# Kernel tuning notes

Hardware: AMD Instinct MI355X
Metric: run time of the kernel (lower is better)

Reference implementation:

```python
import jax, jax.numpy as jnp
import numpy as np

B, S, D, H, E = 2, 2048, 1024, 2048, 8


def setup_inputs() -> dict:
    key = jax.random.key(0)
    ks = jax.random.split(key, 5)
    scale_in = 0.02
    x = jax.random.normal(ks[0], (B, S, D), dtype=jnp.float32)
    Wr = jax.random.normal(ks[1], (D, E), dtype=jnp.float32) * scale_in
    br = jnp.zeros((E,), dtype=jnp.float32)
    W1 = jax.random.normal(ks[2], (E, D, H), dtype=jnp.float32) * (1.0 / np.sqrt(D))
    b1 = jnp.zeros((E, H), dtype=jnp.float32)
    W2 = jax.random.normal(ks[3], (E, H, D), dtype=jnp.float32) * (1.0 / np.sqrt(H))
    b2 = jnp.zeros((E, D), dtype=jnp.float32)
    return {"x": x, "Wr": Wr, "br": br, "W1": W1, "b1": b1, "W2": W2, "b2": b2, "k": 2}


def reference(x, Wr, br, W1, b1, W2, b2, k):
    # Router: top-k logits, softmax over the k selected logits
    logits = x @ Wr + br                       # [B,S,E]
    top_v, top_i = jax.lax.top_k(logits, k)    # [B,S,k]
    scores = jax.nn.softmax(top_v, axis=-1)    # [B,S,k]

    # Dense all-expert MLP (reference combine): [B,S,E,*]
    h = jax.nn.relu(jnp.einsum('bsd,edh->bseh', x, W1) + b1[None, None])
    eo = jnp.einsum('bseh,ehd->bsed', h, W2) + b2[None, None]  # [B,S,E,D]

    # Gather the k selected experts per token and combine with scores
    sel = jnp.take_along_axis(eo, top_i[..., None], axis=2)   # [B,S,k,D]
    out = jnp.sum(scores[..., None] * sel, axis=2)             # [B,S,D]
    return out
```

## Files before the change

kernel.cpp:

```cpp
#include <hip/hip_runtime.h>
#include <hip/hip_bf16.h>

#define TOKENS 4096
#define DDIM 1024
#define HDIM 2048
#define NEXP 8
#define NASSIGN 8192
#define MAX_TILES 80

typedef __attribute__((ext_vector_type(8))) __bf16 bf16x8;
typedef __attribute__((ext_vector_type(4))) float f32x4;
typedef __attribute__((ext_vector_type(4))) unsigned short u16x4;

__device__ __forceinline__ unsigned short f2bf(float f) {
    unsigned int u = __builtin_bit_cast(unsigned int, f);
    u += 0x7fffu + ((u >> 16) & 1u);
    return (unsigned short)(u >> 16);
}

__global__ __launch_bounds__(256) void router_kernel(
    const float* __restrict__ x, const float* __restrict__ Wr, const float* __restrict__ br,
    unsigned short* __restrict__ x_bf, int* __restrict__ topk_e, float* __restrict__ topk_s,
    float* __restrict__ out)
{
    {
        float4* o4 = (float4*)(out + (long)blockIdx.x * 4 * DDIM);
        const float4 z = {0.f, 0.f, 0.f, 0.f};
        for (int i = threadIdx.x; i < DDIM; i += 256) o4[i] = z;
    }
    const int t = blockIdx.x * 4 + (threadIdx.x >> 6);
    const int lane = threadIdx.x & 63;
    const float* xr = x + (long)t * DDIM;
    unsigned short* xo = x_bf + (long)t * DDIM;
    float acc[8] = {0.f,0.f,0.f,0.f,0.f,0.f,0.f,0.f};
    for (int it = 0; it < DDIM / 64; ++it) {
        const int d = it * 64 + lane;
        const float xv = xr[d];
        xo[d] = f2bf(xv);
        const float4 w0 = *(const float4*)(Wr + d * 8);
        const float4 w1 = *(const float4*)(Wr + d * 8 + 4);
        acc[0] += xv * w0.x; acc[1] += xv * w0.y; acc[2] += xv * w0.z; acc[3] += xv * w0.w;
        acc[4] += xv * w1.x; acc[5] += xv * w1.y; acc[6] += xv * w1.z; acc[7] += xv * w1.w;
    }
#pragma unroll
    for (int e = 0; e < 8; ++e) {
        float v = acc[e];
        for (int off = 32; off > 0; off >>= 1) v += __shfl_down(v, off, 64);
        acc[e] = v;
    }
    if (lane == 0) {
        float lg[8];
#pragma unroll
        for (int e = 0; e < 8; ++e) lg[e] = acc[e] + br[e];
        int i0 = 0; float v0 = lg[0];
#pragma unroll
        for (int e = 1; e < 8; ++e) if (lg[e] > v0) { v0 = lg[e]; i0 = e; }
        int i1 = -1; float v1 = -3.4e38f;
#pragma unroll
        for (int e = 0; e < 8; ++e) if (e != i0 && lg[e] > v1) { v1 = lg[e]; i1 = e; }
        const float e1 = expf(v1 - v0);
        const float inv = 1.f / (1.f + e1);
        topk_e[t * 2]     = i0; topk_s[t * 2]     = inv;
        topk_e[t * 2 + 1] = i1; topk_s[t * 2 + 1] = e1 * inv;
    }
}

__global__ __launch_bounds__(1024) void build_lists_kernel(
    const int* __restrict__ topk_e, const float* __restrict__ topk_s,
    int* __restrict__ token_list, float* __restrict__ score_list, int* __restrict__ meta)
{
    __shared__ int cnt[NEXP];
    __shared__ int cur[NEXP];
    const int tid = threadIdx.x;
    const int lane = tid & 63;
    if (tid < NEXP) cnt[tid] = 0;
    __syncthreads();
    {
        int acc = 0;
        for (int it = 0; it < NASSIGN / 1024; ++it) {
            const int e = topk_e[it * 1024 + tid];
#pragma unroll
            for (int ee = 0; ee < NEXP; ++ee) {
                const unsigned long long m = __ballot(e == ee);
                if (lane == ee) acc += __popcll(m);
            }
        }
        if (lane < NEXP) atomicAdd(&cnt[lane], acc);
    }
    __syncthreads();
    if (tid == 0) {
        int accu = 0, ntile = 0;
        for (int e = 0; e < NEXP; ++e) {
            const int c = cnt[e];
            cur[e] = accu;
            for (int r = 0; r * 128 < c; ++r) {
                meta[1 + ntile] = e;
                meta[1 + MAX_TILES + ntile] = accu + r * 128;
                meta[1 + 2 * MAX_TILES + ntile] = (c - r * 128) < 128 ? (c - r * 128) : 128;
                ++ntile;
            }
            accu += c;
        }
        meta[0] = ntile;
    }
    __syncthreads();
    for (int it = 0; it < NASSIGN / 1024; ++it) {
        const int idx = it * 1024 + tid;
        const int e = topk_e[idx];
        const float s = topk_s[idx];
        int pos = 0;
#pragma unroll
        for (int ee = 0; ee < NEXP; ++ee) {
            const unsigned long long m = __ballot(e == ee);
            if (e == ee) {
                const int leader = __ffsll((long long)m) - 1;
                int wbase = 0;
                if (lane == leader) wbase = atomicAdd(&cur[ee], __popcll(m));
                wbase = __shfl(wbase, leader, 64);
                pos = wbase + __popcll(m & ((1ull << lane) - 1ull));
            }
        }
        token_list[pos] = idx >> 1;
        score_list[pos] = s;
    }
}

__global__ __launch_bounds__(256) void transpose_cvt_kernel(
    const float* __restrict__ W1, const float* __restrict__ W2,
    unsigned short* __restrict__ W1t, unsigned short* __restrict__ W2t)
{
    __shared__ unsigned short tile[64 * 68];
    const int z = blockIdx.y;
    const bool is1 = z < 8;
    const int e = is1 ? z : z - 8;
    const int K = is1 ? DDIM : HDIM;
    const int N = is1 ? HDIM : DDIM;
    const float* src = (is1 ? W1 : W2) + (long)e * K * N;
    unsigned short* dst = (is1 ? W1t : W2t) + (long)e * K * N;
    const int ktiles = K >> 6;
    const int k0 = (blockIdx.x % ktiles) * 64;
    const int n0 = (blockIdx.x / ktiles) * 64;
    const int r0 = threadIdx.x >> 4;
    const int c4 = (threadIdx.x & 15) * 4;
#pragma unroll
    for (int i = 0; i < 4; ++i) {
        const int r = r0 + i * 16;
        const float4 v = *(const float4*)(src + (long)(k0 + r) * N + n0 + c4);
        tile[(c4 + 0) * 68 + r] = f2bf(v.x);
        tile[(c4 + 1) * 68 + r] = f2bf(v.y);
        tile[(c4 + 2) * 68 + r] = f2bf(v.z);
        tile[(c4 + 3) * 68 + r] = f2bf(v.w);
    }
    __syncthreads();
#pragma unroll
    for (int i = 0; i < 4; ++i) {
        const int rn = r0 + i * 16;
        u16x4 o;
        o.x = tile[rn * 68 + c4 + 0];
        o.y = tile[rn * 68 + c4 + 1];
        o.z = tile[rn * 68 + c4 + 2];
        o.w = tile[rn * 68 + c4 + 3];
        *(u16x4*)(dst + (long)(n0 + rn) * K + k0 + c4) = o;
    }
}

template<int KDIM, int NDIM, bool G2>
__global__ __launch_bounds__(256, 3) void expert_gemm(
    const unsigned short* __restrict__ Abase,
    const unsigned short* __restrict__ Bt,
    const float* __restrict__ bias,
    unsigned short* __restrict__ Hout,
    float* __restrict__ Out,
    const int* __restrict__ token_list,
    const float* __restrict__ score_list,
    const int* __restrict__ meta)
{
    const int nt = meta[0];
    const int xcd = blockIdx.x & 7;
    const int off = blockIdx.x >> 3;
    const int q = nt >> 3;
    const int r = nt & 7;
    const int cnt_i = q + (xcd < r ? 1 : 0);
    if (off >= cnt_i) return;
    const int t = xcd * q + (xcd < r ? xcd : r) + off;
    const int e = meta[1 + t];
    const int slot0 = meta[1 + MAX_TILES + t];
    const int rows_valid = meta[1 + 2 * MAX_TILES + t];
    const int n0 = blockIdx.y * 128;

    __shared__ unsigned short As[3][128 * 32];
    __shared__ unsigned short Bs[3][128 * 32];

    const int tid = threadIdx.x;
    const int lane = tid & 63;
    const int w = tid >> 6;
    const int wm = w & 1;
    const int wn = w >> 1;
    const int quad = lane >> 4;
    const int l15 = lane & 15;

    const unsigned short* aptr[2];
    const unsigned short* bptr[2];
    int ldsoff[2];
#pragma unroll
    for (int c = 0; c < 2; ++c) {
        const int chunk = c * 256 + tid;
        const int row = chunk >> 2;
        const int kc = (chunk & 3) ^ ((row >> 1) & 3);
        const int rr = row < rows_valid ? row : rows_valid - 1;
        const long arow = G2 ? (long)(slot0 + rr) : (long)token_list[slot0 + rr];
        aptr[c] = Abase + arow * (long)KDIM + kc * 8;
        bptr[c] = Bt + ((long)e * NDIM + n0 + row) * (long)KDIM + kc * 8;
        ldsoff[c] = (c * 256 + w * 64) * 8;
    }

    f32x4 acc[4][4] = {};
    constexpr int NITER = KDIM / 32;

    auto issue = [&](int buf, int k) {
        const int kof = k * 32;
#pragma unroll
        for (int c = 0; c < 2; ++c)
            __builtin_amdgcn_global_load_lds(
                (const __attribute__((address_space(1))) unsigned int*)(aptr[c] + kof),
                (__attribute__((address_space(3))) unsigned int*)&As[buf][ldsoff[c]], 16, 0, 0);
#pragma unroll
        for (int c = 0; c < 2; ++c)
            __builtin_amdgcn_global_load_lds(
                (const __attribute__((address_space(1))) unsigned int*)(bptr[c] + kof),
                (__attribute__((address_space(3))) unsigned int*)&Bs[buf][ldsoff[c]], 16, 0, 0);
    };

    auto compute = [&](int buf) {
        const unsigned short* Ab = As[buf];
        const unsigned short* Bb = Bs[buf];
        const int slot = (quad ^ ((l15 >> 1) & 3)) * 8;
        bf16x8 af[4], bfr[4];
#pragma unroll
        for (int mi = 0; mi < 4; ++mi)
            af[mi] = *(const bf16x8*)&Ab[(wm * 64 + mi * 16 + l15) * 32 + slot];
#pragma unroll
        for (int ni = 0; ni < 4; ++ni)
            bfr[ni] = *(const bf16x8*)&Bb[(wn * 64 + ni * 16 + l15) * 32 + slot];
#pragma unroll
        for (int mi = 0; mi < 4; ++mi)
#pragma unroll
            for (int ni = 0; ni < 4; ++ni)
                acc[mi][ni] = __builtin_amdgcn_mfma_f32_16x16x32_bf16(af[mi], bfr[ni], acc[mi][ni], 0, 0, 0);
    };

    issue(0, 0);
    issue(1, 1);
#pragma unroll 1
    for (int k = 0; k < NITER - 1; ++k) {
        asm volatile("s_waitcnt vmcnt(4)\n\ts_barrier" ::: "memory");
        compute(k % 3);
        asm volatile("s_barrier" ::: "memory");
        if (k + 2 < NITER) issue((k + 2) % 3, k + 2);
    }
    asm volatile("s_waitcnt vmcnt(0)\n\ts_barrier" ::: "memory");
    compute((NITER - 1) % 3);

#pragma unroll
    for (int mi = 0; mi < 4; ++mi) {
#pragma unroll
        for (int ni = 0; ni < 4; ++ni) {
            const int col = n0 + wn * 64 + ni * 16 + l15;
#pragma unroll
            for (int rr = 0; rr < 4; ++rr) {
                const int row = wm * 64 + mi * 16 + quad * 4 + rr;
                if (row < rows_valid) {
                    float v = acc[mi][ni][rr] + bias[e * NDIM + col];
                    if (!G2) {
                        v = v > 0.f ? v : 0.f;
                        Hout[(long)(slot0 + row) * NDIM + col] = f2bf(v);
                    } else {
                        const int slot = slot0 + row;
                        const int tok = token_list[slot];
                        const float s = score_list[slot];
                        unsafeAtomicAdd(&Out[(long)tok * NDIM + col], s * v);
                    }
                }
            }
        }
    }
}

extern "C" void kernel_launch(void* const* d_in, const int* in_sizes, int n_in,
                              void* d_out, int out_size, void* d_ws, size_t ws_size,
                              hipStream_t stream)
{
    (void)in_sizes; (void)n_in; (void)out_size; (void)ws_size;
    const float* x  = (const float*)d_in[0];
    const float* Wr = (const float*)d_in[1];
    const float* br = (const float*)d_in[2];
    const float* W1 = (const float*)d_in[3];
    const float* b1 = (const float*)d_in[4];
    const float* W2 = (const float*)d_in[5];
    const float* b2 = (const float*)d_in[6];
    float* out = (float*)d_out;

    char* ws = (char*)d_ws;
    unsigned short* x_bf  = (unsigned short*)(ws);
    unsigned short* W1t   = (unsigned short*)(ws + 8388608);
    unsigned short* W2t   = (unsigned short*)(ws + 41943040);
    unsigned short* hbuf  = (unsigned short*)(ws + 75497472);
    int*   topk_e     = (int*)(ws + 109051904);
    float* topk_s     = (float*)(ws + 109084672);
    int*   token_list = (int*)(ws + 109117440);
    float* score_list = (float*)(ws + 109150208);
    int*   meta       = (int*)(ws + 109182976);

    router_kernel<<<TOKENS / 4, 256, 0, stream>>>(x, Wr, br, x_bf, topk_e, topk_s, out);
    build_lists_kernel<<<1, 1024, 0, stream>>>(topk_e, topk_s, token_list, score_list, meta);
    transpose_cvt_kernel<<<dim3(512, 16), 256, 0, stream>>>(W1, W2, W1t, W2t);
    expert_gemm<DDIM, HDIM, false><<<dim3(MAX_TILES, HDIM / 128), 256, 0, stream>>>(
        x_bf, W1t, b1, hbuf, nullptr, token_list, score_list, meta);
    expert_gemm<HDIM, DDIM, true><<<dim3(MAX_TILES, DDIM / 128), 256, 0, stream>>>(
        hbuf, W2t, b2, nullptr, out, token_list, score_list, meta);
}
```

Baseline: 356.2 us.

## Register-staged double-buffered GEMM loads and split routing list build into scan plus scatter

```diff
diff --git a/kernel.cpp b/kernel.cpp
--- a/kernel.cpp
+++ b/kernel.cpp
@@ -11,6 +11,7 @@
 typedef __attribute__((ext_vector_type(8))) __bf16 bf16x8;
 typedef __attribute__((ext_vector_type(4))) float f32x4;
 typedef __attribute__((ext_vector_type(4))) unsigned short u16x4;
+typedef __attribute__((ext_vector_type(4))) int i32x4;
 
 __device__ __forceinline__ unsigned short f2bf(float f) {
     unsigned int u = __builtin_bit_cast(unsigned int, f);
@@ -65,34 +66,30 @@
     }
 }
 
-__global__ __launch_bounds__(1024) void build_lists_kernel(
-    const int* __restrict__ topk_e, const float* __restrict__ topk_s,
-    int* __restrict__ token_list, float* __restrict__ score_list, int* __restrict__ meta)
+__global__ __launch_bounds__(256) void scan_kernel(
+    const int* __restrict__ topk_e, int* __restrict__ meta)
 {
     __shared__ int cnt[NEXP];
-    __shared__ int cur[NEXP];
     const int tid = threadIdx.x;
     const int lane = tid & 63;
     if (tid < NEXP) cnt[tid] = 0;
     __syncthreads();
-    {
-        int acc = 0;
-        for (int it = 0; it < NASSIGN / 1024; ++it) {
-            const int e = topk_e[it * 1024 + tid];
-#pragma unroll
-            for (int ee = 0; ee < NEXP; ++ee) {
-                const unsigned long long m = __ballot(e == ee);
-                if (lane == ee) acc += __popcll(m);
-            }
-        }
-        if (lane < NEXP) atomicAdd(&cnt[lane], acc);
-    }
+    int acc = 0;
+    for (int it = 0; it < NASSIGN / 256; ++it) {
+        const int e = topk_e[it * 256 + tid];
+#pragma unroll
+        for (int ee = 0; ee < NEXP; ++ee) {
+            const unsigned long long m = __ballot(e == ee);
+            if (lane == ee) acc += __popcll(m);
+        }
+    }
+    if (lane < NEXP) atomicAdd(&cnt[lane], acc);
     __syncthreads();
     if (tid == 0) {
         int accu = 0, ntile = 0;
         for (int e = 0; e < NEXP; ++e) {
             const int c = cnt[e];
-            cur[e] = accu;
+            meta[256 + e] = accu;
             for (int r = 0; r * 128 < c; ++r) {
                 meta[1 + ntile] = e;
                 meta[1 + MAX_TILES + ntile] = accu + r * 128;
@@ -103,26 +100,30 @@
         }
         meta[0] = ntile;
     }
-    __syncthreads();
-    for (int it = 0; it < NASSIGN / 1024; ++it) {
-        const int idx = it * 1024 + tid;
-        const int e = topk_e[idx];
-        const float s = topk_s[idx];
-        int pos = 0;
-#pragma unroll
-        for (int ee = 0; ee < NEXP; ++ee) {
-            const unsigned long long m = __ballot(e == ee);
-            if (e == ee) {
-                const int leader = __ffsll((long long)m) - 1;
-                int wbase = 0;
-                if (lane == leader) wbase = atomicAdd(&cur[ee], __popcll(m));
-                wbase = __shfl(wbase, leader, 64);
-                pos = wbase + __popcll(m & ((1ull << lane) - 1ull));
-            }
-        }
-        token_list[pos] = idx >> 1;
-        score_list[pos] = s;
-    }
+}
+
+__global__ __launch_bounds__(256) void scatter_kernel(
+    const int* __restrict__ topk_e, const float* __restrict__ topk_s,
+    int* __restrict__ meta, int* __restrict__ token_list, float* __restrict__ score_list)
+{
+    const int idx = blockIdx.x * 256 + threadIdx.x;
+    const int lane = threadIdx.x & 63;
+    const int e = topk_e[idx];
+    const float s = topk_s[idx];
+    int pos = 0;
+#pragma unroll
+    for (int ee = 0; ee < NEXP; ++ee) {
+        const unsigned long long m = __ballot(e == ee);
+        if (e == ee) {
+            const int leader = __ffsll((long long)m) - 1;
+            int wbase = 0;
+            if (lane == leader) wbase = atomicAdd(&meta[256 + ee], __popcll(m));
+            wbase = __shfl(wbase, leader, 64);
+            pos = wbase + __popcll(m & ((1ull << lane) - 1ull));
+        }
+    }
+    token_list[pos] = idx >> 1;
+    score_list[pos] = s;
 }
 
 __global__ __launch_bounds__(256) void transpose_cvt_kernel(
@@ -188,8 +189,8 @@
     const int rows_valid = meta[1 + 2 * MAX_TILES + t];
     const int n0 = blockIdx.y * 128;
 
-    __shared__ unsigned short As[3][128 * 32];
-    __shared__ unsigned short Bs[3][128 * 32];
+    __shared__ unsigned short As[2][128 * 32];
+    __shared__ unsigned short Bs[2][128 * 32];
 
     const int tid = threadIdx.x;
     const int lane = tid & 63;
@@ -201,7 +202,7 @@
 
     const unsigned short* aptr[2];
     const unsigned short* bptr[2];
-    int ldsoff[2];
+    int ldsaddr[2];
 #pragma unroll
     for (int c = 0; c < 2; ++c) {
         const int chunk = c * 256 + tid;
@@ -211,25 +212,32 @@
         const long arow = G2 ? (long)(slot0 + rr) : (long)token_list[slot0 + rr];
         aptr[c] = Abase + arow * (long)KDIM + kc * 8;
         bptr[c] = Bt + ((long)e * NDIM + n0 + row) * (long)KDIM + kc * 8;
-        ldsoff[c] = (c * 256 + w * 64) * 8;
+        ldsaddr[c] = chunk * 8;
     }
 
     f32x4 acc[4][4] = {};
     constexpr int NITER = KDIM / 32;
 
-    auto issue = [&](int buf, int k) {
-        const int kof = k * 32;
-#pragma unroll
-        for (int c = 0; c < 2; ++c)
-            __builtin_amdgcn_global_load_lds(
-                (const __attribute__((address_space(1))) unsigned int*)(aptr[c] + kof),
-                (__attribute__((address_space(3))) unsigned int*)&As[buf][ldsoff[c]], 16, 0, 0);
-#pragma unroll
-        for (int c = 0; c < 2; ++c)
-            __builtin_amdgcn_global_load_lds(
-                (const __attribute__((address_space(1))) unsigned int*)(bptr[c] + kof),
-                (__attribute__((address_space(3))) unsigned int*)&Bs[buf][ldsoff[c]], 16, 0, 0);
-    };
+    i32x4 ga[2][2], gb[2][2];
+
+#define LOAD_STAGE(s, k)                                                        \
+    {                                                                           \
+        const long kof = (long)(k) * 32;                                        \
+        ga[s][0] = *(const i32x4*)(aptr[0] + kof);                              \
+        ga[s][1] = *(const i32x4*)(aptr[1] + kof);                              \
+        gb[s][0] = *(const i32x4*)(bptr[0] + kof);                              \
+        gb[s][1] = *(const i32x4*)(bptr[1] + kof);                              \
+    }
+
+#define WRITE_STAGE(buf, s)                                                     \
+    {                                                                           \
+        *(i32x4*)&As[buf][ldsaddr[0]] = ga[s][0];                               \
+        *(i32x4*)&As[buf][ldsaddr[1]] = ga[s][1];                               \
+        *(i32x4*)&Bs[buf][ldsaddr[0]] = gb[s][0];                               \
+        *(i32x4*)&Bs[buf][ldsaddr[1]] = gb[s][1];                               \
+    }
+
+#define LGKM_BARRIER() asm volatile("s_waitcnt lgkmcnt(0)\n\ts_barrier" ::: "memory")
 
     auto compute = [&](int buf) {
         const unsigned short* Ab = As[buf];
@@ -249,17 +257,35 @@
                 acc[mi][ni] = __builtin_amdgcn_mfma_f32_16x16x32_bf16(af[mi], bfr[ni], acc[mi][ni], 0, 0, 0);
     };
 
-    issue(0, 0);
-    issue(1, 1);
+    LOAD_STAGE(0, 0);
+    LOAD_STAGE(1, 1);
+    WRITE_STAGE(0, 0);
+    LGKM_BARRIER();
+
 #pragma unroll 1
-    for (int k = 0; k < NITER - 1; ++k) {
-        asm volatile("s_waitcnt vmcnt(4)\n\ts_barrier" ::: "memory");
-        compute(k % 3);
-        asm volatile("s_barrier" ::: "memory");
-        if (k + 2 < NITER) issue((k + 2) % 3, k + 2);
-    }
-    asm volatile("s_waitcnt vmcnt(0)\n\ts_barrier" ::: "memory");
-    compute((NITER - 1) % 3);
+    for (int k2 = 0; k2 < NITER / 2; ++k2) {
+        {
+            const int k = 2 * k2;
+            compute(0);
+            LGKM_BARRIER();
+            WRITE_STAGE(1, 1);
+            if (k + 2 < NITER) LOAD_STAGE(0, k + 2);
+            LGKM_BARRIER();
+        }
+        {
+            const int k = 2 * k2 + 1;
+            compute(1);
+            if (k + 1 < NITER) {
+                LGKM_BARRIER();
+                WRITE_STAGE(0, 0);
+                if (k + 2 < NITER) LOAD_STAGE(1, k + 2);
+                LGKM_BARRIER();
+            }
+        }
+    }
+#undef LOAD_STAGE
+#undef WRITE_STAGE
+#undef LGKM_BARRIER
 
 #pragma unroll
     for (int mi = 0; mi < 4; ++mi) {
@@ -312,7 +338,8 @@
     int*   meta       = (int*)(ws + 109182976);
 
     router_kernel<<<TOKENS / 4, 256, 0, stream>>>(x, Wr, br, x_bf, topk_e, topk_s, out);
-    build_lists_kernel<<<1, 1024, 0, stream>>>(topk_e, topk_s, token_list, score_list, meta);
+    scan_kernel<<<1, 256, 0, stream>>>(topk_e, meta);
+    scatter_kernel<<<NASSIGN / 256, 256, 0, stream>>>(topk_e, topk_s, meta, token_list, score_list);
     transpose_cvt_kernel<<<dim3(512, 16), 256, 0, stream>>>(W1, W2, W1t, W2t);
     expert_gemm<DDIM, HDIM, false><<<dim3(MAX_TILES, HDIM / 128), 256, 0, stream>>>(
         x_bf, W1t, b1, hbuf, nullptr, token_list, score_list, meta);
```

Result: no change. 362.8 us (+1.8%).
